# Kernel optimization log

Measured on AMD Instinct MI355X. Metric: run time of the kernel, lower is better.

Reference implementation:

```python
import jax, jax.numpy as jnp
import numpy as np

ACT_BITS = 8
Q_B = 2 ** (ACT_BITS - 1)          # 128
EPS = 1e-6                          # module epsilon
GN_EPS = 1e-5                       # torch GroupNorm default eps
SCALE = 0.01                        # fixed ternary weight scale (buffer)
STRIDE = 1
PADDING = 1


def setup_inputs() -> dict:
    key = jax.random.key(0)
    k1, k2 = jax.random.split(key)
    x = jax.random.normal(k1, (16, 256, 64, 64), dtype=jnp.float32)
    weight = jax.random.normal(k2, (256, 256, 3, 3), dtype=jnp.float32)
    bias = jnp.zeros((256,), dtype=jnp.float32)
    ln_weight = jnp.ones((256,), dtype=jnp.float32)
    ln_bias = jnp.zeros((256,), dtype=jnp.float32)
    return {"x": x, "weight": weight, "bias": bias,
            "ln_weight": ln_weight, "ln_bias": ln_bias}


def _group_norm_1group(x, gamma, beta):
    # GroupNorm(1, C): normalize over (C, H, W) per sample, per-channel affine.
    mean = jnp.mean(x, axis=(1, 2, 3), keepdims=True)
    var = jnp.var(x, axis=(1, 2, 3), keepdims=True)
    xn = (x - mean) * jax.lax.rsqrt(var + GN_EPS)
    return xn * gamma[None, :, None, None] + beta[None, :, None, None]


def reference(x, weight, bias, ln_weight, ln_bias):
    # 1) GroupNorm
    x_ln = _group_norm_1group(x, ln_weight, ln_bias)

    # 2) BitNet absmax activation quantization (global absmax)
    gamma = jnp.maximum(jnp.max(jnp.abs(x_ln)), EPS)
    x_scaled = x_ln * (Q_B / gamma)
    x_clipped = jnp.clip(x_scaled, -Q_B + EPS, Q_B - EPS)
    x_quant = jnp.round(x_clipped)

    # 3) Ternary weight quantization with fixed scale: {-SCALE, 0, +SCALE}
    delta = 0.7 * jnp.mean(jnp.abs(weight))  # TTQ threshold
    w_q = jnp.where(weight > delta, SCALE,
                    jnp.where(weight < -delta, -SCALE, 0.0)).astype(weight.dtype)

    # 4) Conv2d (NCHW, OIHW)
    y = jax.lax.conv_general_dilated(
        x_quant, w_q,
        window_strides=(STRIDE, STRIDE),
        padding=[(PADDING, PADDING), (PADDING, PADDING)],
        dimension_numbers=("NCHW", "OIHW", "NCHW"),
        feature_group_count=1,
    )

    # 5) Dequant + bias
    y = y * (gamma / Q_B) + bias[None, :, None, None]
    return y
```

## Files before the change

kernel.cpp:

```cpp
#include <hip/hip_runtime.h>
#include <hip/hip_bf16.h>

#define CHW   1048576
#define XQ_BYTES 17842176u
#define WQ_OFF   17842176u
#define GNP_OFF  18432000u
#define CMM_OFF  18448384u
#define MR_OFF   18481152u
#define SC_OFF   18481280u
#define WP_OFF   18481296u
#define DL_OFF   18481584u
#define EVC_OFF  18481588u
#define EVL_OFF  18481592u

typedef __attribute__((ext_vector_type(4)))  int i32x4;
typedef __attribute__((ext_vector_type(16))) int i32x16;

__device__ __forceinline__ void gload16(const void* g, void* l) {
    __builtin_amdgcn_global_load_lds(
        (const __attribute__((address_space(1))) unsigned int*)(unsigned long long)(g),
        (__attribute__((address_space(3))) unsigned int*)(unsigned int)(unsigned long long)(l),
        16, 0, 0);
}

__global__ void k_pass1(const float* __restrict__ x, double2* __restrict__ part,
                        float2* __restrict__ cmm) {
    int bid = blockIdx.x;
    int n = bid >> 6, c4 = bid & 63;
    int t = threadIdx.x, ch = t >> 6, lane = t & 63;
    int c = c4 * 4 + ch;
    const float4* p = (const float4*)(x + (size_t)n * CHW + (size_t)c * 4096);
    double s = 0.0, ss = 0.0;
    float mn = 1e30f, mx = -1e30f;
#pragma unroll
    for (int k = 0; k < 16; ++k) {
        float4 v = p[k * 64 + lane];
        mn = fminf(mn, fminf(fminf(v.x, v.y), fminf(v.z, v.w)));
        mx = fmaxf(mx, fmaxf(fmaxf(v.x, v.y), fmaxf(v.z, v.w)));
        double dx = v.x, dy = v.y, dz = v.z, dw = v.w;
        s  += dx + dy + dz + dw;
        ss += dx * dx + dy * dy + dz * dz + dw * dw;
    }
    for (int o = 32; o; o >>= 1) {
        s += __shfl_down(s, o); ss += __shfl_down(ss, o);
        mn = fminf(mn, __shfl_down(mn, o)); mx = fmaxf(mx, __shfl_down(mx, o));
    }
    __shared__ double sh0[4], sh1[4];
    if (lane == 0) {
        cmm[n * 256 + c] = make_float2(mn, mx);
        sh0[ch] = s; sh1[ch] = ss;
    }
    __syncthreads();
    if (t == 0)
        part[bid] = make_double2(sh0[0] + sh0[1] + sh0[2] + sh0[3],
                                 sh1[0] + sh1[1] + sh1[2] + sh1[3]);
}

__global__ void k_wsum(const float* __restrict__ w, double* __restrict__ wp) {
    int blk = blockIdx.x, t = threadIdx.x;
    const float4* p = (const float4*)(w + (size_t)blk * 16384);
    double s = 0.0;
#pragma unroll
    for (int j = 0; j < 16; ++j) {
        float4 v = p[j * 256 + t];
        s += fabs((double)v.x) + fabs((double)v.y) + fabs((double)v.z) + fabs((double)v.w);
    }
    for (int o = 32; o; o >>= 1) s += __shfl_down(s, o);
    __shared__ double sh[4];
    if ((t & 63) == 0) sh[t >> 6] = s;
    __syncthreads();
    if (t == 0) wp[blk] = sh[0] + sh[1] + sh[2] + sh[3];
}

__global__ void k_scalars(const double2* __restrict__ part, const float2* __restrict__ cmm,
                          const float* __restrict__ lnw, const float* __restrict__ lnb,
                          const double* __restrict__ wp,
                          float2* __restrict__ mr, float* __restrict__ sc,
                          float* __restrict__ dl, int* __restrict__ evcnt) {
    __shared__ float shm[16], shr[16];
    int t = threadIdx.x;
    {
        int n = t >> 4, i = t & 15;
        double s = 0.0, ss = 0.0;
#pragma unroll
        for (int k = 0; k < 4; ++k) {
            double2 v = part[n * 64 + i * 4 + k];
            s += v.x; ss += v.y;
        }
        for (int o = 8; o; o >>= 1) { s += __shfl_down(s, o); ss += __shfl_down(ss, o); }
        if (i == 0) {
            double mean = s * (1.0 / 1048576.0);
            double var  = ss * (1.0 / 1048576.0) - mean * mean;
            shm[n] = (float)mean; shr[n] = (float)(1.0 / sqrt(var + 1e-5));
        }
    }
    __syncthreads();
    if (t < 16) mr[t] = make_float2(shm[t], shr[t]);
    if (t == 0) evcnt[0] = 0;
    float m = 0.0f;
#pragma unroll
    for (int k = 0; k < 16; ++k) {
        int idx = t + k * 256;
        int n = idx >> 8, c = idx & 255;
        float2 v = cmm[idx];
        float scale = lnw[c] * shr[n];
        float shift = lnb[c] - shm[n] * scale;
        m = fmaxf(m, fmaxf(fabsf(v.x * scale + shift), fabsf(v.y * scale + shift)));
    }
    for (int o = 32; o; o >>= 1) m = fmaxf(m, __shfl_down(m, o));
    __shared__ float shg[4];
    if ((t & 63) == 0) shg[t >> 6] = m;
    __syncthreads();
    if (t == 0) {
        float gamma = fmaxf(fmaxf(fmaxf(shg[0], shg[1]), fmaxf(shg[2], shg[3])), 1e-6f);
        sc[0] = gamma;
        sc[1] = 128.0f / gamma;
        sc[2] = (gamma / 128.0f) * 0.01f;
    }
    if (t < 64) {
        double s = (t < 36) ? wp[t] : 0.0;
        for (int o = 32; o; o >>= 1) s += __shfl_down(s, o);
        if (t == 0) dl[0] = (float)(0.7 * (s / 589824.0));
    }
}

__global__ void k_wquant(const float* __restrict__ w, const float* __restrict__ dl,
                         signed char* __restrict__ wq) {
    __shared__ float sw[2304];
    int co = blockIdx.x, t = threadIdx.x;
    const float* wr = w + (size_t)co * 2304;
#pragma unroll
    for (int j = 0; j < 9; ++j) sw[j * 256 + t] = wr[j * 256 + t];
    __syncthreads();
    float d = dl[0];
#pragma unroll
    for (int tap = 0; tap < 9; ++tap) {
        float v = sw[t * 9 + tap];
        int s = (v > d) ? 1 : ((v < -d) ? -1 : 0);
        wq[tap * 65536 + co * 256 + t] = (signed char)s;
    }
}

__global__ void k_halo(unsigned char* __restrict__ xq) {
    int idx = blockIdx.x * 8 + (threadIdx.x >> 5);
    int n = idx / 260, p = idx - n * 260;
    int hh, ww;
    if (p < 66)       { hh = 0;        ww = p; }
    else if (p < 132) { hh = 65;       ww = p - 66; }
    else if (p < 196) { hh = p - 131;  ww = 0; }
    else              { hh = p - 195;  ww = 65; }
    *(uint2*)(xq + ((size_t)(n * 66 + hh) * 66 + ww) * 256 + (threadIdx.x & 31) * 8) =
        make_uint2(0, 0);
}

__global__ void k_quantx(const float* __restrict__ x, const float2* __restrict__ mr,
                         const float* __restrict__ sc, const float* __restrict__ lnw,
                         const float* __restrict__ lnb, unsigned char* __restrict__ xq,
                         int* __restrict__ evcnt, int* __restrict__ evlist) {
    int bid = blockIdx.x;
    int n = bid >> 6, hg = (bid >> 2) & 15, cg = bid & 3;
    int t = threadIdx.x;
    int w = t & 63, h = hg * 4 + (t >> 6);
    float2 m = mr[n];
    float s128 = sc[1];
    uint u[16];
    const float* xp = x + (((size_t)n * 256 + cg * 64) * 64 + h) * 64 + w;
#pragma unroll
    for (int ci = 0; ci < 64; ++ci) {
        int c = cg * 64 + ci;
        float g = lnw[c] * m.y;
        float be = lnb[c];
        float v = xp[(size_t)ci * 4096];
        float xs = ((v - m.x) * g + be) * s128;
        xs = fminf(fmaxf(xs, -(128.0f - 1e-6f)), 128.0f - 1e-6f);
        int q = (int)rintf(xs);
        if (q == 128) {
            int idx = atomicAdd(evcnt, 1);
            if (idx < 1024) evlist[idx] = (n << 20) | (h << 14) | (w << 8) | c;
            q = 127;
        }
        uint b = (uint)(q & 255);
        if ((ci & 3) == 0) u[ci >> 2] = b; else u[ci >> 2] |= b << ((ci & 3) * 8);
    }
    unsigned char* op = xq + ((size_t)(n * 66 + h + 1) * 66 + (w + 1)) * 256 + cg * 64;
    uint4* o4 = (uint4*)op;
#pragma unroll
    for (int s2 = 0; s2 < 4; ++s2)
        o4[s2] = make_uint4(u[s2 * 4], u[s2 * 4 + 1], u[s2 * 4 + 2], u[s2 * 4 + 3]);
}

__global__ void k_fix(const signed char* __restrict__ wq, const int* __restrict__ evcnt,
                      const int* __restrict__ evlist, const float* __restrict__ sc,
                      float* __restrict__ out) {
    int cnt = *evcnt; if (cnt > 1024) cnt = 1024;
    float qs = sc[2];
    int co = threadIdx.x;
    for (int e = blockIdx.x; e < cnt; e += gridDim.x) {
        int pk = evlist[e];
        int n = pk >> 20, h = (pk >> 14) & 63, w = (pk >> 8) & 63, ci = pk & 255;
#pragma unroll
        for (int ty = 0; ty < 3; ++ty)
#pragma unroll
            for (int tx = 0; tx < 3; ++tx) {
                int i = h + 1 - ty, j = w + 1 - tx;
                if (i < 0 || i > 63 || j < 0 || j > 63) continue;
                int sgn = wq[(ty * 3 + tx) * 65536 + co * 256 + ci];
                if (sgn)
                    atomicAdd(out + (((size_t)n * 256 + co) * 64 + i) * 64 + j,
                              qs * (float)sgn);
            }
    }
}

#define ABUF  16384
#define BBASE 49152
#define LD16(off) (*(const i32x4*)&lds8[(off)])
#define MFMA_I8(A, B, C) __builtin_amdgcn_mfma_i32_32x32x32_i8(A, B, C, 0, 0, 0)

#define STAGE_A(AS) { \
    const int _so = (AS) * ABUF + wv * 1024; \
    gload16(aSrc + stA,         lds8 + _so); \
    gload16(aSrc + stA + 33792, lds8 + _so + 8192); \
    if (aKc < 3) { aKc++; stA += 64; } \
    else { aKc = 0; if (aTx < 2) { aTx++; stA += 64; } else { aTx = 0; stA += 16192; } } }

#define STAGE_B(BS) { \
    const int _so = BBASE + (BS) * ABUF + wv * 1024; \
    gload16(bSrc + stB,         lds8 + _so); \
    gload16(bSrc + stB + 32768, lds8 + _so + 8192); \
    if (bKc < 3) { bKc++; stB += 64; } else { bKc = 0; stB += 65344; } }

#define ITER(AR, BR, AS, BS, DOA, DOB, W) { \
    const int _ab = (AR) * ABUF; \
    const int _bb = BBASE + (BR) * ABUF; \
    if (DOB) STAGE_B(BS) \
    if (DOA) STAGE_A(AS) \
    i32x4 b00 = LD16(_bb + rdB);          i32x4 b01 = LD16((_bb + rdB) ^ 32); \
    i32x4 b10 = LD16(_bb + rdB + 2048);   i32x4 b11 = LD16((_bb + rdB + 2048) ^ 32); \
    _Pragma("unroll") \
    for (int _m = 0; _m < 4; ++_m) { \
        const int _ra = _ab + rdA + _m * 2048; \
        i32x4 a0 = LD16(_ra); \
        i32x4 a1 = LD16(_ra ^ 32); \
        __builtin_amdgcn_s_setprio(1); \
        acc[_m][0] = MFMA_I8(a0, b00, acc[_m][0]); \
        acc[_m][1] = MFMA_I8(a0, b10, acc[_m][1]); \
        acc[_m][0] = MFMA_I8(a1, b01, acc[_m][0]); \
        acc[_m][1] = MFMA_I8(a1, b11, acc[_m][1]); \
        __builtin_amdgcn_s_setprio(0); \
    } \
    if ((W) == 2)      { asm volatile("s_waitcnt vmcnt(2)" ::: "memory"); } \
    else if ((W) == 0) { asm volatile("s_waitcnt vmcnt(0)" ::: "memory"); } \
    __builtin_amdgcn_s_barrier(); \
    __builtin_amdgcn_sched_barrier(0); \
}

#define STORE4(P, A, BV) { \
    float4 v0; v0.x = (float)(A)[0]*qs+(BV);  v0.y = (float)(A)[1]*qs+(BV);  v0.z = (float)(A)[2]*qs+(BV);  v0.w = (float)(A)[3]*qs+(BV);  *(float4*)((P))      = v0; \
    float4 v1; v1.x = (float)(A)[4]*qs+(BV);  v1.y = (float)(A)[5]*qs+(BV);  v1.z = (float)(A)[6]*qs+(BV);  v1.w = (float)(A)[7]*qs+(BV);  *(float4*)((P) + 8)  = v1; \
    float4 v2; v2.x = (float)(A)[8]*qs+(BV);  v2.y = (float)(A)[9]*qs+(BV);  v2.z = (float)(A)[10]*qs+(BV); v2.w = (float)(A)[11]*qs+(BV); *(float4*)((P) + 16) = v2; \
    float4 v3; v3.x = (float)(A)[12]*qs+(BV); v3.y = (float)(A)[13]*qs+(BV); v3.z = (float)(A)[14]*qs+(BV); v3.w = (float)(A)[15]*qs+(BV); *(float4*)((P) + 24) = v3; }

__global__ __launch_bounds__(512, 2) void k_conv(const unsigned char* __restrict__ xq,
                                                 const signed char* __restrict__ wq,
                                                 const float* __restrict__ sc,
                                                 const float* __restrict__ bias,
                                                 float* __restrict__ out) {
    __shared__ __align__(128) unsigned char lds8[81920];
    int t = threadIdx.x, wv = t >> 6, l = t & 63;
    int wm = wv >> 2, wn = wv & 3;
    int l31 = l & 31, l5 = l >> 5;

    int bid = ((int)blockIdx.x & 7) * 32 + ((int)blockIdx.x >> 3);
    int n = bid >> 4, h2 = (bid & 15) << 2;

    int s_src = (l & 7) ^ (l >> 3);
    int sb2   = (s_src >> 2) & 1;
    int skc   = s_src & 3;
    int RA    = wv * 16 + ((l >> 3) << 1) + sb2;
    int hsub  = RA >> 6, wA = RA & 63;
    const unsigned char* aSrc = xq +
        ((size_t)(n * 66 + h2 + hsub) * 66 + wA) * 256 + skc * 16;
    int coB = ((wv * 8 + (l >> 3)) << 1) + sb2;
    const unsigned char* bSrc = (const unsigned char*)wq + (size_t)coB * 256 + skc * 16;

    int q3    = (l31 >> 1) & 7;
    int s0    = ((l31 & 1) << 2) | l5;
    int phys0 = s0 ^ q3;
    int rdA = (wm * 64 + (l31 >> 1)) * 128 + phys0 * 16;
    int rdB = (wn * 32 + (l31 >> 1)) * 128 + phys0 * 16;

    i32x16 acc[4][2] = {};

    int stA = 0, aKc = 0, aTx = 0;
    int stB = 0, bKc = 0;
    STAGE_A(0)
    STAGE_B(0)
    STAGE_A(1)
    asm volatile("s_waitcnt vmcnt(2)" ::: "memory");
    __builtin_amdgcn_s_barrier();
    __builtin_amdgcn_sched_barrier(0);

#pragma unroll 1
    for (int it = 0; it < 5; ++it) {
        ITER(0, 0, 2, 1, 1, 1, 2)
        ITER(1, 1, 0, 0, 1, 1, 2)
        ITER(2, 0, 1, 1, 1, 1, 2)
        ITER(0, 1, 2, 0, 1, 1, 2)
        ITER(1, 0, 0, 1, 1, 1, 2)
        ITER(2, 1, 1, 0, 1, 1, 2)
    }
    ITER(0, 0, 2, 1, 1, 1, 2)
    ITER(1, 1, 0, 0, 1, 1, 2)
    ITER(2, 0, 1, 1, 1, 1, 2)
    ITER(0, 1, 2, 0, 1, 1, 2)
    ITER(1, 0, 0, 1, 0, 1, 0)
    ITER(2, 1, 0, 0, 0, 0, -1)

    float qs = sc[2];
#pragma unroll
    for (int m = 0; m < 4; ++m) {
        int h = h2 + wm * 2 + (m >> 1);
        int wb = (m & 1) * 32 + l5 * 4;
        size_t obase = (size_t)n * CHW + (size_t)h * 64 + wb;
#pragma unroll
        for (int nf = 0; nf < 2; ++nf) {
            int co = wn * 64 + nf * 32 + l31;
            float bv = bias[co];
            float* ob = out + obase + (size_t)co * 4096;
            STORE4(ob, acc[m][nf], bv)
        }
    }
}

extern "C" void kernel_launch(void* const* d_in, const int* in_sizes, int n_in,
                              void* d_out, int out_size, void* d_ws, size_t ws_size,
                              hipStream_t stream) {
    (void)in_sizes; (void)n_in; (void)out_size; (void)ws_size;
    const float* x    = (const float*)d_in[0];
    const float* wgt  = (const float*)d_in[1];
    const float* bias = (const float*)d_in[2];
    const float* lnw  = (const float*)d_in[3];
    const float* lnb  = (const float*)d_in[4];
    float* out = (float*)d_out;
    char* ws = (char*)d_ws;

    unsigned char* xq  = (unsigned char*)ws;
    signed char*   wq  = (signed char*)(ws + WQ_OFF);
    double2* gnp = (double2*)(ws + GNP_OFF);
    float2*  cmm = (float2*)(ws + CMM_OFF);
    float2*  mr  = (float2*)(ws + MR_OFF);
    float*   sc  = (float*)(ws + SC_OFF);
    double*  wp  = (double*)(ws + WP_OFF);
    float*   dl  = (float*)(ws + DL_OFF);
    int*     evc = (int*)(ws + EVC_OFF);
    int*     evl = (int*)(ws + EVL_OFF);

    k_pass1  <<<1024, 256, 0, stream>>>(x, gnp, cmm);
    k_wsum   <<<36,   256, 0, stream>>>(wgt, wp);
    k_scalars<<<1,    256, 0, stream>>>(gnp, cmm, lnw, lnb, wp, mr, sc, dl, evc);
    k_wquant <<<256,  256, 0, stream>>>(wgt, dl, wq);
    k_halo   <<<520,  256, 0, stream>>>(xq);
    k_quantx <<<1024, 256, 0, stream>>>(x, mr, sc, lnw, lnb, xq, evc, evl);
    k_conv   <<<256,  512, 0, stream>>>(xq, wq, sc, bias, out);
    k_fix    <<<64,   256, 0, stream>>>(wq, evc, evl, sc, out);
}
```

Baseline: 106.1 us.

## Deepen conv K-loop pipeline to 5 stages with two K-steps per barrier

The implicit-GEMM int8 conv loop moves from a 3-stage A / 2-stage B LDS ring to a unified 5-slot ring, each slot holding A and B together. Every iteration now issues loads for two future stages and runs two K-steps of MFMAs between barriers. This halves the barrier count and keeps more global loads in flight. LDS use grows from 80 KB to 160 KB per block, which likely drops occupancy from 2 blocks per CU to 1 despite the launch bound of 2.

```diff
diff --git a/kernel.cpp b/kernel.cpp
--- a/kernel.cpp
+++ b/kernel.cpp
@@ -212,29 +212,26 @@
     }
 }
 
-#define ABUF  16384
-#define BBASE 49152
+#define ABUFB 32768
 #define LD16(off) (*(const i32x4*)&lds8[(off)])
 #define MFMA_I8(A, B, C) __builtin_amdgcn_mfma_i32_32x32x32_i8(A, B, C, 0, 0, 0)
 
 #define STAGE_A(AS) { \
-    const int _so = (AS) * ABUF + wv * 1024; \
+    const int _so = (AS) * ABUFB + wv * 1024; \
     gload16(aSrc + stA,         lds8 + _so); \
     gload16(aSrc + stA + 33792, lds8 + _so + 8192); \
     if (aKc < 3) { aKc++; stA += 64; } \
     else { aKc = 0; if (aTx < 2) { aTx++; stA += 64; } else { aTx = 0; stA += 16192; } } }
 
 #define STAGE_B(BS) { \
-    const int _so = BBASE + (BS) * ABUF + wv * 1024; \
+    const int _so = (BS) * ABUFB + 16384 + wv * 1024; \
     gload16(bSrc + stB,         lds8 + _so); \
     gload16(bSrc + stB + 32768, lds8 + _so + 8192); \
     if (bKc < 3) { bKc++; stB += 64; } else { bKc = 0; stB += 65344; } }
 
-#define ITER(AR, BR, AS, BS, DOA, DOB, W) { \
-    const int _ab = (AR) * ABUF; \
-    const int _bb = BBASE + (BR) * ABUF; \
-    if (DOB) STAGE_B(BS) \
-    if (DOA) STAGE_A(AS) \
+#define STEP(R) { \
+    const int _ab = (R) * ABUFB; \
+    const int _bb = (R) * ABUFB + 16384; \
     i32x4 b00 = LD16(_bb + rdB);          i32x4 b01 = LD16((_bb + rdB) ^ 32); \
     i32x4 b10 = LD16(_bb + rdB + 2048);   i32x4 b11 = LD16((_bb + rdB + 2048) ^ 32); \
     _Pragma("unroll") \
@@ -248,11 +245,16 @@
         acc[_m][0] = MFMA_I8(a1, b01, acc[_m][0]); \
         acc[_m][1] = MFMA_I8(a1, b11, acc[_m][1]); \
         __builtin_amdgcn_s_setprio(0); \
-    } \
-    if ((W) == 2)      { asm volatile("s_waitcnt vmcnt(2)" ::: "memory"); } \
+    } }
+
+#define PITER(R0, R1, S0, S1, DO0, DO1, W) { \
+    if (DO0) { STAGE_A(S0) STAGE_B(S0) } \
+    if (DO1) { STAGE_A(S1) STAGE_B(S1) } \
+    STEP(R0) \
+    STEP(R1) \
+    if ((W) == 4)      { asm volatile("s_waitcnt vmcnt(4)" ::: "memory"); } \
     else if ((W) == 0) { asm volatile("s_waitcnt vmcnt(0)" ::: "memory"); } \
-    __builtin_amdgcn_s_barrier(); \
-    __builtin_amdgcn_sched_barrier(0); \
+    if ((W) >= 0) { __builtin_amdgcn_s_barrier(); __builtin_amdgcn_sched_barrier(0); } \
 }
 
 #define STORE4(P, A, BV) { \
@@ -266,7 +268,7 @@
                                                  const float* __restrict__ sc,
                                                  const float* __restrict__ bias,
                                                  float* __restrict__ out) {
-    __shared__ __align__(128) unsigned char lds8[81920];
+    __shared__ __align__(128) unsigned char lds8[163840];
     int t = threadIdx.x, wv = t >> 6, l = t & 63;
     int wm = wv >> 2, wn = wv & 3;
     int l31 = l & 31, l5 = l >> 5;
@@ -294,28 +296,24 @@
 
     int stA = 0, aKc = 0, aTx = 0;
     int stB = 0, bKc = 0;
-    STAGE_A(0)
-    STAGE_B(0)
-    STAGE_A(1)
-    asm volatile("s_waitcnt vmcnt(2)" ::: "memory");
+    STAGE_A(0) STAGE_B(0)
+    STAGE_A(1) STAGE_B(1)
+    STAGE_A(2) STAGE_B(2)
+    asm volatile("s_waitcnt vmcnt(4)" ::: "memory");
     __builtin_amdgcn_s_barrier();
     __builtin_amdgcn_sched_barrier(0);
 
 #pragma unroll 1
-    for (int it = 0; it < 5; ++it) {
-        ITER(0, 0, 2, 1, 1, 1, 2)
-        ITER(1, 1, 0, 0, 1, 1, 2)
-        ITER(2, 0, 1, 1, 1, 1, 2)
-        ITER(0, 1, 2, 0, 1, 1, 2)
-        ITER(1, 0, 0, 1, 1, 1, 2)
-        ITER(2, 1, 1, 0, 1, 1, 2)
-    }
-    ITER(0, 0, 2, 1, 1, 1, 2)
-    ITER(1, 1, 0, 0, 1, 1, 2)
-    ITER(2, 0, 1, 1, 1, 1, 2)
-    ITER(0, 1, 2, 0, 1, 1, 2)
-    ITER(1, 0, 0, 1, 0, 1, 0)
-    ITER(2, 1, 0, 0, 0, 0, -1)
+    for (int it = 0; it < 3; ++it) {
+        PITER(0, 1, 3, 4, 1, 1, 4)
+        PITER(2, 3, 0, 1, 1, 1, 4)
+        PITER(4, 0, 2, 3, 1, 1, 4)
+        PITER(1, 2, 4, 0, 1, 1, 4)
+        PITER(3, 4, 1, 2, 1, 1, 4)
+    }
+    PITER(0, 1, 3, 4, 1, 1, 4)
+    PITER(2, 3, 0, 0, 1, 0, 0)
+    PITER(4, 0, 0, 0, 0, 0, -1)
 
     float qs = sc[2];
 #pragma unroll
```

Result: no change. 105.1 us (-1.0%).
